# Optimization experiments

Measured on AMD Instinct MI355X. Metric: run time of the kernel, lower is better.

The kernel has to match this reference:

```python
import jax, jax.numpy as jnp
import numpy as np

L, H, D, HD, DFF, V, S, B = 12, 12, 768, 64, 3072, 50257, 512, 4
NEG = -1e10  # mask value used by the torch module (applied incl. diagonal, pre-scale)


def layer_norm(x, g, b, eps=1e-5):
    u = jnp.mean(x, axis=-1, keepdims=True)
    v = jnp.mean((x - u) ** 2, axis=-1, keepdims=True)  # biased variance
    return g * (x - u) / jnp.sqrt(v + eps) + b


def setup_inputs() -> dict:
    key = jax.random.key(0)
    ks = jax.random.split(key, 10)
    f = lambda k, s: 0.02 * jax.random.normal(k, s, dtype=jnp.float32)
    return {
        "tokens": jax.random.randint(ks[0], (B, S), 0, V),
        "E": f(ks[1], (V, D)),
        "P": f(ks[2], (S, D)),
        "Wq": f(ks[3], (L, H, HD, D)),
        "Wk": f(ks[4], (L, H, HD, D)),
        "Wv": f(ks[5], (L, H, HD, D)),
        "Wo": f(ks[6], (L, D, D)),
        "bo": jnp.zeros((L, D), jnp.float32),
        "g1": jnp.ones((L, D), jnp.float32),
        "b1": jnp.zeros((L, D), jnp.float32),
        "g2": jnp.ones((L, D), jnp.float32),
        "b2": jnp.zeros((L, D), jnp.float32),
        "W1": f(ks[7], (L, DFF, D)),
        "bff1": jnp.zeros((L, DFF), jnp.float32),
        "W2": f(ks[8], (L, D, DFF)),
        "bff2": jnp.zeros((L, D), jnp.float32),
        "gf": jnp.ones((D,), jnp.float32),
        "bf": jnp.zeros((D,), jnp.float32),
    }


def reference(tokens, E, P, Wq, Wk, Wv, Wo, bo, g1, b1, g2, b2, W1, bff1, W2, bff2, gf, bf):
    x = E[tokens] + P[None, :, :]  # [B,S,D]; embed_dropout is identity at eval
    # Faithful mask: triu with diagonal=0 (masks the diagonal too), added BEFORE 1/sqrt(dk)
    mask = jnp.triu(jnp.ones((S, S), jnp.float32), k=0) * NEG
    scale = 1.0 / jnp.sqrt(jnp.float32(HD))
    for l in range(L):
        h = layer_norm(x, g1[l], b1[l])
        Q = jnp.einsum('bsd,hkd->bhsk', h, Wq[l])
        K = jnp.einsum('bsd,hkd->bhsk', h, Wk[l])
        Vh = jnp.einsum('bsd,hkd->bhsk', h, Wv[l])
        sc = (jnp.einsum('bhqk,bhmk->bhqm', Q, K) + mask) * scale  # [B,H,S,S]
        A = jax.nn.softmax(sc, axis=-1)
        o = jnp.einsum('bhqm,bhmk->bhqk', A, Vh)  # [B,H,S,HD]
        o = o.transpose(0, 2, 1, 3).reshape(B, S, D)  # concat heads
        x = x + jnp.einsum('bsd,ed->bse', o, Wo[l]) + bo[l]
        h2 = layer_norm(x, g2[l], b2[l])
        ff = jax.nn.gelu(jnp.einsum('bsd,fd->bsf', h2, W1[l]) + bff1[l], approximate=False)
        x = x + jnp.einsum('bsf,df->bsd', ff, W2[l]) + bff2[l]
    x = layer_norm(x, gf, bf)
    return jnp.einsum('bsd,vd->bsv', x, E)  # weight-tied LM head
```

## Files before the change

kernel.cpp:

```cpp
#include <hip/hip_runtime.h>
#include <hip/hip_bf16.h>
#include <math.h>
#include <stdint.h>

#define L      12
#define H      12
#define DMODEL 768
#define HDIM   64
#define DFF    3072
#define VOCAB  50257
#define VPAD2  50432
#define SEQ    512
#define BATCH  4
#define MTOK   2048
#define BKK    64

typedef __hip_bfloat16 bf16;
typedef __bf16 bf16x8 __attribute__((ext_vector_type(8)));
typedef float  f32x4  __attribute__((ext_vector_type(4)));

__device__ inline unsigned int f2bf_bits(float f) {
    __hip_bfloat16 h = __float2bfloat16(f);
    return (unsigned int)__builtin_bit_cast(unsigned short, h);
}

typedef __attribute__((address_space(1))) unsigned int as1_uint;
typedef __attribute__((address_space(3))) unsigned int as3_uint;

__device__ inline void load_lds_16B(const void* g, void* l) {
    __builtin_amdgcn_global_load_lds((as1_uint*)(uintptr_t)g,
                                     (as3_uint*)(uintptr_t)l, 16, 0, 0);
}

__device__ inline int xcd_swz(int raw, int nwg) {
    return (raw & 7) * (nwg >> 3) + (raw >> 3);
}

struct CvtP {
    const float* src[7];
    bf16* dst[7];
    long ns[7];
    long nt[7];
};

__global__ void cvt_all_kernel(CvtP c) {
    long gid0 = ((long)blockIdx.x * blockDim.x + threadIdx.x) * 8;
    long gstr = (long)gridDim.x * blockDim.x * 8;
    for (int s = 0; s < 7; s++) {
        const float* src = c.src[s];
        bf16* dst = c.dst[s];
        long ns = c.ns[s], ntt = c.nt[s];
        for (long i8 = gid0; i8 < ntt; i8 += gstr) {
            uint4 out;
            if (i8 < ns) {
                float4 a = *reinterpret_cast<const float4*>(src + i8);
                float4 b = *reinterpret_cast<const float4*>(src + i8 + 4);
                out.x = f2bf_bits(a.x) | (f2bf_bits(a.y) << 16);
                out.y = f2bf_bits(a.z) | (f2bf_bits(a.w) << 16);
                out.z = f2bf_bits(b.x) | (f2bf_bits(b.y) << 16);
                out.w = f2bf_bits(b.z) | (f2bf_bits(b.w) << 16);
            } else {
                out = (uint4){0u, 0u, 0u, 0u};
            }
            *reinterpret_cast<uint4*>(dst + i8) = out;
        }
    }
}

__global__ __launch_bounds__(256) void embed_ln_kernel(
        float* __restrict__ x, bf16* __restrict__ hout,
        const int* __restrict__ tok, const float* __restrict__ E,
        const float* __restrict__ Pp, const float* __restrict__ g,
        const float* __restrict__ b) {
    int wave = threadIdx.x >> 6, lane = threadIdx.x & 63;
    int row = blockIdx.x * 4 + wave;
    int s = row & (SEQ - 1);
    long ebase = (long)tok[row] * 192;
    const float4* E4 = (const float4*)E;
    const float4* P4 = (const float4*)Pp;
    float4 v[3];
    float s1 = 0.f, s2 = 0.f;
    #pragma unroll
    for (int e = 0; e < 3; e++) {
        int c4 = e * 64 + lane;
        float4 a = E4[ebase + c4];
        float4 p = P4[s * 192 + c4];
        a.x += p.x; a.y += p.y; a.z += p.z; a.w += p.w;
        v[e] = a;
        ((float4*)x)[(size_t)row * 192 + c4] = a;
        s1 += a.x + a.y + a.z + a.w;
        s2 += a.x * a.x + a.y * a.y + a.z * a.z + a.w * a.w;
    }
    #pragma unroll
    for (int o = 32; o > 0; o >>= 1) {
        s1 += __shfl_xor(s1, o);
        s2 += __shfl_xor(s2, o);
    }
    float u    = s1 * (1.f / DMODEL);
    float var  = s2 * (1.f / DMODEL) - u * u;
    float rstd = rsqrtf(var + 1e-5f);
    #pragma unroll
    for (int e = 0; e < 3; e++) {
        int c4 = e * 64 + lane;
        float4 gg = ((const float4*)g)[c4];
        float4 bb = ((const float4*)b)[c4];
        float y0 = gg.x * (v[e].x - u) * rstd + bb.x;
        float y1 = gg.y * (v[e].y - u) * rstd + bb.y;
        float y2 = gg.z * (v[e].z - u) * rstd + bb.z;
        float y3 = gg.w * (v[e].w - u) * rstd + bb.w;
        uint2 o2;
        o2.x = f2bf_bits(y0) | (f2bf_bits(y1) << 16);
        o2.y = f2bf_bits(y2) | (f2bf_bits(y3) << 16);
        ((uint2*)hout)[(size_t)row * 192 + c4] = o2;
    }
}

__global__ __launch_bounds__(256) void reduce_ln_kernel(
        float* __restrict__ x, const float* __restrict__ part, int S,
        const float* __restrict__ bias, const float* __restrict__ g,
        const float* __restrict__ b, bf16* __restrict__ hout) {
    int wave = threadIdx.x >> 6, lane = threadIdx.x & 63;
    int row = blockIdx.x * 4 + wave;
    const float4* part4 = (const float4*)part;
    float4 v[3];
    float s1 = 0.f, s2 = 0.f;
    #pragma unroll
    for (int e = 0; e < 3; e++) {
        int c4 = e * 64 + lane;
        size_t idx = (size_t)row * 192 + c4;
        float4 a = ((const float4*)x)[idx];
        float4 bi = ((const float4*)bias)[c4];
        a.x += bi.x; a.y += bi.y; a.z += bi.z; a.w += bi.w;
        for (int sl = 0; sl < S; sl++) {
            float4 p = part4[((size_t)sl * MTOK + row) * 192 + c4];
            a.x += p.x; a.y += p.y; a.z += p.z; a.w += p.w;
        }
        v[e] = a;
        ((float4*)x)[idx] = a;
        s1 += a.x + a.y + a.z + a.w;
        s2 += a.x * a.x + a.y * a.y + a.z * a.z + a.w * a.w;
    }
    #pragma unroll
    for (int o = 32; o > 0; o >>= 1) {
        s1 += __shfl_xor(s1, o);
        s2 += __shfl_xor(s2, o);
    }
    float u    = s1 * (1.f / DMODEL);
    float var  = s2 * (1.f / DMODEL) - u * u;
    float rstd = rsqrtf(var + 1e-5f);
    #pragma unroll
    for (int e = 0; e < 3; e++) {
        int c4 = e * 64 + lane;
        float4 gg = ((const float4*)g)[c4];
        float4 bb = ((const float4*)b)[c4];
        float y0 = gg.x * (v[e].x - u) * rstd + bb.x;
        float y1 = gg.y * (v[e].y - u) * rstd + bb.y;
        float y2 = gg.z * (v[e].z - u) * rstd + bb.z;
        float y3 = gg.w * (v[e].w - u) * rstd + bb.w;
        uint2 o2;
        o2.x = f2bf_bits(y0) | (f2bf_bits(y1) << 16);
        o2.y = f2bf_bits(y2) | (f2bf_bits(y3) << 16);
        ((uint2*)hout)[(size_t)row * 192 + c4] = o2;
    }
}

#define BM 128

template<int BN_, int EPI>
__global__ __launch_bounds__(256) void gemm_bt(
    const bf16* __restrict__ A, const bf16* __restrict__ Bmat, long strideBz,
    void* __restrict__ Cout, long strideCz,
    const float* __restrict__ bias,
    int Mm, int Nn, int Kk, int Nstore, int kslice)
{
    constexpr int NF = BN_ / 32;
    __shared__ __align__(16) bf16 As[2][BM * BKK];
    __shared__ __align__(16) bf16 Bs[2][BN_ * BKK];
    int tid = threadIdx.x;
    int lane = tid & 63, wave = tid >> 6;

    int Mtiles = Mm / BM;
    int id = xcd_swz(blockIdx.x, gridDim.x);
    int bm = (id % Mtiles) * BM;
    int bn = (id / Mtiles) * BN_;
    int z = blockIdx.z;
    const bf16* Bz = Bmat + (size_t)z * strideBz;
    int wr = (wave >> 1) * 64, wc = (wave & 1) * (BN_ / 2);

    int k0 = (EPI == 4) ? z * kslice : 0;
    int nt = ((EPI == 4) ? kslice : Kk) / BKK;

    f32x4 acc[4][NF];
    #pragma unroll
    for (int i = 0; i < 4; i++)
        #pragma unroll
        for (int j = 0; j < NF; j++) acc[i][j] = (f32x4){0.f, 0.f, 0.f, 0.f};

    auto stage = [&](int slot, int kt) {
        #pragma unroll
        for (int i = 0; i < 4; i++) {
            int byte = i * 4096 + tid * 16;
            int r = byte >> 7;
            int scb = (byte & 127) ^ ((r & 7) << 4);
            load_lds_16B(A + (size_t)(bm + r) * Kk + kt + (scb >> 1),
                         (char*)As[slot] + byte);
        }
        #pragma unroll
        for (int i = 0; i < BN_ / 32; i++) {
            int byte = i * 4096 + tid * 16;
            int r = byte >> 7;
            int scb = (byte & 127) ^ ((r & 7) << 4);
            load_lds_16B(Bz + (size_t)(bn + r) * Kk + kt + (scb >> 1),
                         (char*)Bs[slot] + byte);
        }
    };

    const int swz_rd = (lane & 7) << 4;
    stage(0, k0);
    for (int t = 0; t < nt; ++t) {
        if (t + 1 < nt) {
            stage((t + 1) & 1, k0 + (t + 1) * BKK);
            if constexpr (BN_ == 128) {
                asm volatile("s_waitcnt vmcnt(8)" ::: "memory");
            } else {
                asm volatile("s_waitcnt vmcnt(6)" ::: "memory");
            }
        } else {
            asm volatile("s_waitcnt vmcnt(0)" ::: "memory");
        }
        __builtin_amdgcn_s_barrier();
        __builtin_amdgcn_sched_barrier(0);
        __builtin_amdgcn_s_setprio(1);
        int cur = t & 1;
        #pragma unroll
        for (int kk = 0; kk < 2; ++kk) {
            bf16x8 af[4], bfr[NF];
            int ro = lane & 15;
            int cob = kk * 64 + (lane >> 4) * 16;
            #pragma unroll
            for (int mi = 0; mi < 4; mi++) {
                int row = wr + mi * 16 + ro;
                af[mi] = *reinterpret_cast<const bf16x8*>(
                    (const char*)As[cur] + row * 128 + (cob ^ swz_rd));
            }
            #pragma unroll
            for (int ni = 0; ni < NF; ni++) {
                int row = wc + ni * 16 + ro;
                bfr[ni] = *reinterpret_cast<const bf16x8*>(
                    (const char*)Bs[cur] + row * 128 + (cob ^ swz_rd));
            }
            #pragma unroll
            for (int mi = 0; mi < 4; mi++)
                #pragma unroll
                for (int ni = 0; ni < NF; ni++)
                    acc[mi][ni] = __builtin_amdgcn_mfma_f32_16x16x32_bf16(
                        af[mi], bfr[ni], acc[mi][ni], 0, 0, 0);
        }
        __builtin_amdgcn_s_setprio(0);
        __builtin_amdgcn_s_barrier();
    }

    int rbase = bm + wr + ((lane >> 4) << 2);
    int cbase = bn + wc + (lane & 15);
    #pragma unroll
    for (int mi = 0; mi < 4; mi++) {
        #pragma unroll
        for (int ni = 0; ni < NF; ni++) {
            int col = cbase + ni * 16;
            #pragma unroll
            for (int r = 0; r < 4; r++) {
                int row = rbase + mi * 16 + r;
                float v = acc[mi][ni][r];
                if constexpr (EPI == 0) {
                    ((bf16*)Cout)[(size_t)z * strideCz + (size_t)row * Nn + col] =
                        __float2bfloat16(v);
                } else if constexpr (EPI == 2) {
                    float t2 = v + bias[col];
                    float gel = 0.5f * t2 * (1.f + erff(t2 * 0.70710678118654752f));
                    ((bf16*)Cout)[(size_t)row * Nn + col] = __float2bfloat16(gel);
                } else if constexpr (EPI == 3) {
                    if (col < Nstore)
                        ((float*)Cout)[(size_t)row * Nstore + col] = v;
                } else {
                    ((float*)Cout)[(size_t)z * strideCz + (size_t)row * Nn + col] = v;
                }
            }
        }
    }
}

__global__ void __launch_bounds__(512, 2) gemm_head256(
    const bf16* __restrict__ A, const bf16* __restrict__ Bmat,
    float* __restrict__ Cout, int Nstore)
{
    extern __shared__ char smem[];
    const int Kk = DMODEL;
    const int nt = Kk / BKK;
    int tid = threadIdx.x;
    int lane = tid & 63, wave = tid >> 6;
    int wm = wave >> 1, wn = wave & 1;
    int id = xcd_swz(blockIdx.x, gridDim.x);
    int bm = (id & 7) * 256;
    int bn = (id >> 3) * 128;

    f32x4 acc[4][4];
    #pragma unroll
    for (int i = 0; i < 4; i++)
        #pragma unroll
        for (int j = 0; j < 4; j++) acc[i][j] = (f32x4){0.f, 0.f, 0.f, 0.f};

    auto stage = [&](int slot, int kt) {
        #pragma unroll
        for (int i = 0; i < 4; i++) {
            int byte = i * 8192 + tid * 16;
            int r = byte >> 7;
            int scb = (byte & 127) ^ ((r & 7) << 4);
            load_lds_16B(A + (size_t)(bm + r) * Kk + kt + (scb >> 1),
                         smem + slot * 32768 + byte);
        }
        #pragma unroll
        for (int i = 0; i < 2; i++) {
            int byte = i * 8192 + tid * 16;
            int r = byte >> 7;
            int scb = (byte & 127) ^ ((r & 7) << 4);
            load_lds_16B(Bmat + (size_t)(bn + r) * Kk + kt + (scb >> 1),
                         smem + 98304 + slot * 16384 + byte);
        }
    };

    const int swz_rd = (lane & 7) << 4;
    stage(0, 0);
    stage(1, BKK);
    for (int t = 0; t < nt; ++t) {
        if (t < nt - 1) {
            asm volatile("s_waitcnt vmcnt(6)" ::: "memory");
        } else {
            asm volatile("s_waitcnt vmcnt(0)" ::: "memory");
        }
        __builtin_amdgcn_s_barrier();
        __builtin_amdgcn_sched_barrier(0);
        if (t + 2 < nt) stage((t + 2) % 3, (t + 2) * BKK);
        int cur = t % 3;
        const char* Ab = smem + cur * 32768;
        const char* Bb = smem + 98304 + cur * 16384;
        __builtin_amdgcn_s_setprio(1);
        #pragma unroll
        for (int kk = 0; kk < 2; ++kk) {
            bf16x8 af[4], bfr[4];
            int ro = lane & 15;
            int cob = kk * 64 + (lane >> 4) * 16;
            #pragma unroll
            for (int mi = 0; mi < 4; mi++) {
                int row = wm * 64 + mi * 16 + ro;
                af[mi] = *reinterpret_cast<const bf16x8*>(
                    Ab + row * 128 + (cob ^ swz_rd));
            }
            #pragma unroll
            for (int ni = 0; ni < 4; ni++) {
                int row = wn * 64 + ni * 16 + ro;
                bfr[ni] = *reinterpret_cast<const bf16x8*>(
                    Bb + row * 128 + (cob ^ swz_rd));
            }
            #pragma unroll
            for (int mi = 0; mi < 4; mi++)
                #pragma unroll
                for (int ni = 0; ni < 4; ni++)
                    acc[mi][ni] = __builtin_amdgcn_mfma_f32_16x16x32_bf16(
                        af[mi], bfr[ni], acc[mi][ni], 0, 0, 0);
        }
        __builtin_amdgcn_s_setprio(0);
    }

    int rbase = bm + wm * 64 + ((lane >> 4) << 2);
    int cbase = bn + wn * 64 + (lane & 15);
    #pragma unroll
    for (int mi = 0; mi < 4; mi++) {
        #pragma unroll
        for (int ni = 0; ni < 4; ni++) {
            int col = cbase + ni * 16;
            #pragma unroll
            for (int r = 0; r < 4; r++) {
                int row = rbase + mi * 16 + r;
                if (col < Nstore)
                    Cout[(size_t)row * Nstore + col] = acc[mi][ni][r];
            }
        }
    }
}

#define NEGMASK -1e10f
#define SM_SCALE 0.125f

__global__ __launch_bounds__(256) void attn_kernel(
    bf16* __restrict__ o, const bf16* __restrict__ qb,
    const bf16* __restrict__ kb, const bf16* __restrict__ vb)
{
    __shared__ __align__(16) bf16 K_lds[64 * 64];
    __shared__ __align__(16) bf16 VT_lds[64 * 64];
    __shared__ __align__(16) bf16 P_lds[4][16 * 64];

    int tid = threadIdx.x;
    int wave = tid >> 6, lane = tid & 63;
    int g = lane >> 4;
    int cq = lane & 15;
    int idx = xcd_swz(blockIdx.x, gridDim.x);
    int qt = idx & 7;
    int bh = idx >> 3;
    int h = bh % H, b = bh / H;
    int q0 = qt * 64;
    const size_t base = ((size_t)b * SEQ) * DMODEL + h * HDIM;

    bf16x8 qa[2];
    #pragma unroll
    for (int kk = 0; kk < 2; kk++)
        qa[kk] = *reinterpret_cast<const bf16x8*>(
            qb + base + (size_t)(q0 + wave * 16 + cq) * DMODEL + kk * 32 + g * 8);

    f32x4 acc_o[4];
    #pragma unroll
    for (int df = 0; df < 4; df++) acc_o[df] = (f32x4){0.f, 0.f, 0.f, 0.f};
    float m_run[4] = {-INFINITY, -INFINITY, -INFINITY, -INFINITY};
    float l_run[4] = {0.f, 0.f, 0.f, 0.f};

    int ntiles = (qt == 0) ? (SEQ / 64) : (qt + 1);
    for (int t = 0; t < ntiles; ++t) {
        int mt = t * 64;
        __syncthreads();
        #pragma unroll
        for (int i = 0; i < 2; i++) {
            int byte = i * 4096 + tid * 16;
            int r = byte >> 7;
            int scb = (byte & 127) ^ ((r & 7) << 4);
            load_lds_16B(kb + base + (size_t)(mt + r) * DMODEL + (scb >> 1),
                         (char*)K_lds + byte);
        }
        {
            int rp = tid & 31;
            int c0 = (tid >> 5) * 8;
            const bf16* v0p = vb + base + (size_t)(mt + 2 * rp) * DMODEL + c0;
            uint4 a = *reinterpret_cast<const uint4*>(v0p);
            uint4 bb = *reinterpret_cast<const uint4*>(v0p + DMODEL);
            unsigned int au[4] = {a.x, a.y, a.z, a.w};
            unsigned int bu[4] = {bb.x, bb.y, bb.z, bb.w};
            #pragma unroll
            for (int j = 0; j < 8; j++) {
                unsigned int lo = (j & 1) ? (au[j >> 1] >> 16) : (au[j >> 1] & 0xffffu);
                unsigned int hi = (j & 1) ? (bu[j >> 1] >> 16) : (bu[j >> 1] & 0xffffu);
                int d = c0 + j;
                int byte = d * 128 + ((rp * 4) ^ ((d & 7) << 4));
                *reinterpret_cast<unsigned int*>((char*)VT_lds + byte) = lo | (hi << 16);
            }
        }
        __syncthreads();

        f32x4 s[4];
        #pragma unroll
        for (int nf = 0; nf < 4; nf++) s[nf] = (f32x4){0.f, 0.f, 0.f, 0.f};
        __builtin_amdgcn_s_setprio(1);
        #pragma unroll
        for (int kk = 0; kk < 2; kk++) {
            #pragma unroll
            for (int nf = 0; nf < 4; nf++) {
                int row = nf * 16 + cq;
                bf16x8 kf = *reinterpret_cast<const bf16x8*>(
                    (const char*)K_lds + row * 128 +
                    ((kk * 64 + g * 16) ^ ((row & 7) << 4)));
                s[nf] = __builtin_amdgcn_mfma_f32_16x16x32_bf16(qa[kk], kf, s[nf], 0, 0, 0);
            }
        }
        __builtin_amdgcn_s_setprio(0);

        float p[4][4];
        #pragma unroll
        for (int r = 0; r < 4; r++) {
            int qg = q0 + wave * 16 + (g << 2) + r;
            float sv[4];
            float vmax = -INFINITY;
            #pragma unroll
            for (int nf = 0; nf < 4; nf++) {
                int kv = mt + nf * 16 + cq;
                float d = s[nf][r];
                sv[nf] = (kv >= qg) ? (d + NEGMASK) * SM_SCALE : d * SM_SCALE;
                vmax = fmaxf(vmax, sv[nf]);
            }
            vmax = fmaxf(vmax, __shfl_xor(vmax, 1));
            vmax = fmaxf(vmax, __shfl_xor(vmax, 2));
            vmax = fmaxf(vmax, __shfl_xor(vmax, 4));
            vmax = fmaxf(vmax, __shfl_xor(vmax, 8));
            float nm = fmaxf(m_run[r], vmax);
            float f = __expf(m_run[r] - nm);
            m_run[r] = nm;
            float ps = 0.f;
            #pragma unroll
            for (int nf = 0; nf < 4; nf++) {
                float pv = __expf(sv[nf] - nm);
                p[nf][r] = pv;
                ps += pv;
            }
            ps += __shfl_xor(ps, 1);
            ps += __shfl_xor(ps, 2);
            ps += __shfl_xor(ps, 4);
            ps += __shfl_xor(ps, 8);
            l_run[r] = l_run[r] * f + ps;
            #pragma unroll
            for (int df = 0; df < 4; df++) acc_o[df][r] *= f;
        }

        #pragma unroll
        for (int nf = 0; nf < 4; nf++)
            #pragma unroll
            for (int r = 0; r < 4; r++) {
                int q = (g << 2) + r;
                int blog = nf * 32 + cq * 2;
                int byte = wave * 2048 + q * 128 + (blog ^ ((q & 7) << 4));
                *reinterpret_cast<unsigned short*>((char*)P_lds + byte) =
                    (unsigned short)f2bf_bits(p[nf][r]);
            }
        __syncthreads();

        __builtin_amdgcn_s_setprio(1);
        #pragma unroll
        for (int kk = 0; kk < 2; kk++) {
            bf16x8 pa = *reinterpret_cast<const bf16x8*>(
                (const char*)P_lds + wave * 2048 + cq * 128 +
                ((kk * 64 + g * 16) ^ ((cq & 7) << 4)));
            #pragma unroll
            for (int df = 0; df < 4; df++) {
                int row = df * 16 + cq;
                bf16x8 vf = *reinterpret_cast<const bf16x8*>(
                    (const char*)VT_lds + row * 128 +
                    ((kk * 64 + g * 16) ^ ((row & 7) << 4)));
                acc_o[df] = __builtin_amdgcn_mfma_f32_16x16x32_bf16(pa, vf, acc_o[df], 0, 0, 0);
            }
        }
        __builtin_amdgcn_s_setprio(0);
    }

    #pragma unroll
    for (int r = 0; r < 4; r++) {
        float inv = 1.f / l_run[r];
        int qg = q0 + wave * 16 + (g << 2) + r;
        #pragma unroll
        for (int df = 0; df < 4; df++) {
            o[base + (size_t)qg * DMODEL + df * 16 + cq] =
                __float2bfloat16(acc_o[df][r] * inv);
        }
    }
}

extern "C" void kernel_launch(void* const* d_in, const int* in_sizes, int n_in,
                              void* d_out, int out_size, void* d_ws, size_t ws_size,
                              hipStream_t stream)
{
    (void)in_sizes; (void)n_in; (void)out_size; (void)ws_size;
    const int*   tokens = (const int*)d_in[0];
    const float* E    = (const float*)d_in[1];
    const float* P    = (const float*)d_in[2];
    const float* Wq   = (const float*)d_in[3];
    const float* Wk   = (const float*)d_in[4];
    const float* Wv   = (const float*)d_in[5];
    const float* Wo   = (const float*)d_in[6];
    const float* bo   = (const float*)d_in[7];
    const float* g1   = (const float*)d_in[8];
    const float* b1   = (const float*)d_in[9];
    const float* g2   = (const float*)d_in[10];
    const float* b2   = (const float*)d_in[11];
    const float* W1   = (const float*)d_in[12];
    const float* bff1 = (const float*)d_in[13];
    const float* W2   = (const float*)d_in[14];
    const float* bff2 = (const float*)d_in[15];
    const float* gf   = (const float*)d_in[16];
    const float* bfin = (const float*)d_in[17];

    char* ws = (char*)d_ws;
    size_t off = 0;
    auto alloc = [&](size_t bytes) -> void* {
        void* p = ws + off;
        off += (bytes + 255) & ~(size_t)255;
        return p;
    };
    float* x     = (float*)alloc((size_t)MTOK * DMODEL * 4);
    bf16* hbuf   = (bf16*)alloc((size_t)MTOK * DMODEL * 2);
    bf16* qkv    = (bf16*)alloc((size_t)3 * MTOK * DMODEL * 2);
    bf16* obuf   = (bf16*)alloc((size_t)MTOK * DMODEL * 2);
    bf16* ffb    = (bf16*)alloc((size_t)MTOK * DFF * 2);
    float* part  = (float*)alloc((size_t)3 * MTOK * DMODEL * 4);
    bf16* Eb     = (bf16*)alloc((size_t)VPAD2 * DMODEL * 2);
    bf16* Wqkv_b = (bf16*)alloc((size_t)3 * L * DMODEL * DMODEL * 2);
    bf16* Wo_b   = (bf16*)alloc((size_t)L * DMODEL * DMODEL * 2);
    bf16* W1_b   = (bf16*)alloc((size_t)L * DFF * DMODEL * 2);
    bf16* W2_b   = (bf16*)alloc((size_t)L * DMODEL * DFF * 2);

    long nW = (long)L * DMODEL * DMODEL;
    long nF = (long)L * DFF * DMODEL;
    CvtP cp;
    cp.src[0] = E;  cp.dst[0] = Eb;          cp.ns[0] = (long)VOCAB * DMODEL; cp.nt[0] = (long)VPAD2 * DMODEL;
    cp.src[1] = Wq; cp.dst[1] = Wqkv_b;      cp.ns[1] = nW; cp.nt[1] = nW;
    cp.src[2] = Wk; cp.dst[2] = Wqkv_b + nW; cp.ns[2] = nW; cp.nt[2] = nW;
    cp.src[3] = Wv; cp.dst[3] = Wqkv_b + 2 * nW; cp.ns[3] = nW; cp.nt[3] = nW;
    cp.src[4] = Wo; cp.dst[4] = Wo_b;        cp.ns[4] = nW; cp.nt[4] = nW;
    cp.src[5] = W1; cp.dst[5] = W1_b;        cp.ns[5] = nF; cp.nt[5] = nF;
    cp.src[6] = W2; cp.dst[6] = W2_b;        cp.ns[6] = nF; cp.nt[6] = nF;
    cvt_all_kernel<<<2048, 256, 0, stream>>>(cp);

    embed_ln_kernel<<<MTOK / 4, 256, 0, stream>>>(x, hbuf, tokens, E, P, g1, b1);

    const long pstride = (long)MTOK * DMODEL;
    for (int l = 0; l < L; ++l) {
        gemm_bt<64, 0><<<dim3(192, 1, 3), 256, 0, stream>>>(
            hbuf, Wqkv_b + (size_t)l * DMODEL * DMODEL, nW,
            qkv, pstride, nullptr, MTOK, DMODEL, DMODEL, 0, 0);
        attn_kernel<<<BATCH * H * (SEQ / 64), 256, 0, stream>>>(
            obuf, qkv, qkv + pstride, qkv + 2 * pstride);
        gemm_bt<64, 4><<<dim3(192, 1, 3), 256, 0, stream>>>(
            obuf, Wo_b + (size_t)l * DMODEL * DMODEL, 0,
            part, pstride, nullptr, MTOK, DMODEL, DMODEL, 0, DMODEL / 3);
        reduce_ln_kernel<<<MTOK / 4, 256, 0, stream>>>(
            x, part, 3, bo + l * DMODEL, g2 + l * DMODEL, b2 + l * DMODEL, hbuf);
        gemm_bt<128, 2><<<dim3(16 * 24, 1, 1), 256, 0, stream>>>(
            hbuf, W1_b + (size_t)l * DFF * DMODEL, 0,
            ffb, 0, bff1 + l * DFF, MTOK, DFF, DMODEL, 0, 0);
        gemm_bt<64, 4><<<dim3(192, 1, 3), 256, 0, stream>>>(
            ffb, W2_b + (size_t)l * DMODEL * DFF, 0,
            part, pstride, nullptr, MTOK, DMODEL, DFF, 0, DFF / 3);
        const float* ng = (l < L - 1) ? (g1 + (l + 1) * DMODEL) : gf;
        const float* nb = (l < L - 1) ? (b1 + (l + 1) * DMODEL) : bfin;
        reduce_ln_kernel<<<MTOK / 4, 256, 0, stream>>>(
            x, part, 3, bff2 + l * DMODEL, ng, nb, hbuf);
    }

    (void)hipFuncSetAttribute((const void*)gemm_head256,
        hipFuncAttributeMaxDynamicSharedMemorySize, 147456);
    (void)hipGetLastError();
    gemm_head256<<<dim3(8 * 394), 512, 147456, stream>>>(
        hbuf, Eb, (float*)d_out, VOCAB);
    if (hipGetLastError() != hipSuccess) {
        gemm_bt<128, 3><<<dim3(16 * 394, 1, 1), 256, 0, stream>>>(
            hbuf, Eb, 0, d_out, 0, nullptr, MTOK, VPAD2, DMODEL, VOCAB, 0);
    }
}
```

Baseline: 1.740 ms.

## Interleave LDS reads, global prefetch chunks and MFMA phases in LM-head GEMM

Splits each k-tile of the LM-head GEMM main loop into four phases. Each phase loads a subset of A/B fragments from LDS, issues one chunk of the next stage's global-to-LDS prefetch, then runs half the MFMAs. This spreads memory issue across the compute and lowers fragment register pressure (bfr goes from 4 to 2). In exchange it adds extra workgroup barriers and lgkmcnt waits per tile, which may serialize waves.

```diff
diff --git a/kernel.cpp b/kernel.cpp
--- a/kernel.cpp
+++ b/kernel.cpp
@@ -309,29 +309,46 @@
         #pragma unroll
         for (int j = 0; j < 4; j++) acc[i][j] = (f32x4){0.f, 0.f, 0.f, 0.f};
 
-    auto stage = [&](int slot, int kt) {
-        #pragma unroll
-        for (int i = 0; i < 4; i++) {
-            int byte = i * 8192 + tid * 16;
-            int r = byte >> 7;
-            int scb = (byte & 127) ^ ((r & 7) << 4);
-            load_lds_16B(A + (size_t)(bm + r) * Kk + kt + (scb >> 1),
-                         smem + slot * 32768 + byte);
-        }
-        #pragma unroll
-        for (int i = 0; i < 2; i++) {
-            int byte = i * 8192 + tid * 16;
-            int r = byte >> 7;
-            int scb = (byte & 127) ^ ((r & 7) << 4);
-            load_lds_16B(Bmat + (size_t)(bn + r) * Kk + kt + (scb >> 1),
-                         smem + 98304 + slot * 16384 + byte);
+    auto stage_part = [&](int slot, int kt, int chunk) {
+        if (chunk < 2) {
+            #pragma unroll
+            for (int i = 0; i < 2; i++) {
+                int ii = chunk * 2 + i;
+                int byte = ii * 8192 + tid * 16;
+                int r = byte >> 7;
+                int scb = (byte & 127) ^ ((r & 7) << 4);
+                load_lds_16B(A + (size_t)(bm + r) * Kk + kt + (scb >> 1),
+                             smem + slot * 32768 + byte);
+            }
+        } else {
+            #pragma unroll
+            for (int i = 0; i < 2; i++) {
+                int byte = i * 8192 + tid * 16;
+                int r = byte >> 7;
+                int scb = (byte & 127) ^ ((r & 7) << 4);
+                load_lds_16B(Bmat + (size_t)(bn + r) * Kk + kt + (scb >> 1),
+                             smem + 98304 + slot * 16384 + byte);
+            }
         }
     };
 
     const int swz_rd = (lane & 7) << 4;
-    stage(0, 0);
-    stage(1, BKK);
+    const int ro = lane & 15;
+    stage_part(0, 0, 0); stage_part(0, 0, 1); stage_part(0, 0, 2);
+    stage_part(1, BKK, 0); stage_part(1, BKK, 1); stage_part(1, BKK, 2);
+
     for (int t = 0; t < nt; ++t) {
+        int cur = t % 3;
+        const char* Ab = smem + cur * 32768;
+        const char* Bb = smem + 98304 + cur * 16384;
+        int slot2 = (t + 2) % 3;
+        int kt2 = (t + 2) * BKK;
+        bool pf = (t + 2 < nt);
+
+        bf16x8 af[4], bfr[2];
+        int cob0 = (lane >> 4) * 16;
+        int cob1 = 64 + (lane >> 4) * 16;
+
         if (t < nt - 1) {
             asm volatile("s_waitcnt vmcnt(6)" ::: "memory");
         } else {
@@ -339,35 +356,84 @@
         }
         __builtin_amdgcn_s_barrier();
         __builtin_amdgcn_sched_barrier(0);
-        if (t + 2 < nt) stage((t + 2) % 3, (t + 2) * BKK);
-        int cur = t % 3;
-        const char* Ab = smem + cur * 32768;
-        const char* Bb = smem + 98304 + cur * 16384;
+        #pragma unroll
+        for (int mi = 0; mi < 4; mi++) {
+            int row = wm * 64 + mi * 16 + ro;
+            af[mi] = *reinterpret_cast<const bf16x8*>(Ab + row * 128 + (cob0 ^ swz_rd));
+        }
+        #pragma unroll
+        for (int j = 0; j < 2; j++) {
+            int row = wn * 64 + j * 16 + ro;
+            bfr[j] = *reinterpret_cast<const bf16x8*>(Bb + row * 128 + (cob0 ^ swz_rd));
+        }
+        if (pf) stage_part(slot2, kt2, 0);
+        asm volatile("s_waitcnt lgkmcnt(0)" ::: "memory");
+        __builtin_amdgcn_sched_barrier(0);
         __builtin_amdgcn_s_setprio(1);
         #pragma unroll
-        for (int kk = 0; kk < 2; ++kk) {
-            bf16x8 af[4], bfr[4];
-            int ro = lane & 15;
-            int cob = kk * 64 + (lane >> 4) * 16;
-            #pragma unroll
-            for (int mi = 0; mi < 4; mi++) {
-                int row = wm * 64 + mi * 16 + ro;
-                af[mi] = *reinterpret_cast<const bf16x8*>(
-                    Ab + row * 128 + (cob ^ swz_rd));
-            }
-            #pragma unroll
-            for (int ni = 0; ni < 4; ni++) {
-                int row = wn * 64 + ni * 16 + ro;
-                bfr[ni] = *reinterpret_cast<const bf16x8*>(
-                    Bb + row * 128 + (cob ^ swz_rd));
-            }
-            #pragma unroll
-            for (int mi = 0; mi < 4; mi++)
-                #pragma unroll
-                for (int ni = 0; ni < 4; ni++)
-                    acc[mi][ni] = __builtin_amdgcn_mfma_f32_16x16x32_bf16(
-                        af[mi], bfr[ni], acc[mi][ni], 0, 0, 0);
-        }
+        for (int mi = 0; mi < 4; mi++)
+            #pragma unroll
+            for (int j = 0; j < 2; j++)
+                acc[mi][j] = __builtin_amdgcn_mfma_f32_16x16x32_bf16(
+                    af[mi], bfr[j], acc[mi][j], 0, 0, 0);
+        __builtin_amdgcn_s_setprio(0);
+        __builtin_amdgcn_s_barrier();
+
+        #pragma unroll
+        for (int j = 0; j < 2; j++) {
+            int row = wn * 64 + (2 + j) * 16 + ro;
+            bfr[j] = *reinterpret_cast<const bf16x8*>(Bb + row * 128 + (cob0 ^ swz_rd));
+        }
+        if (pf) stage_part(slot2, kt2, 1);
+        asm volatile("s_waitcnt lgkmcnt(0)" ::: "memory");
+        __builtin_amdgcn_sched_barrier(0);
+        __builtin_amdgcn_s_setprio(1);
+        #pragma unroll
+        for (int mi = 0; mi < 4; mi++)
+            #pragma unroll
+            for (int j = 0; j < 2; j++)
+                acc[mi][2 + j] = __builtin_amdgcn_mfma_f32_16x16x32_bf16(
+                    af[mi], bfr[j], acc[mi][2 + j], 0, 0, 0);
+        __builtin_amdgcn_s_setprio(0);
+        __builtin_amdgcn_s_barrier();
+
+        #pragma unroll
+        for (int mi = 0; mi < 4; mi++) {
+            int row = wm * 64 + mi * 16 + ro;
+            af[mi] = *reinterpret_cast<const bf16x8*>(Ab + row * 128 + (cob1 ^ swz_rd));
+        }
+        #pragma unroll
+        for (int j = 0; j < 2; j++) {
+            int row = wn * 64 + j * 16 + ro;
+            bfr[j] = *reinterpret_cast<const bf16x8*>(Bb + row * 128 + (cob1 ^ swz_rd));
+        }
+        if (pf) stage_part(slot2, kt2, 2);
+        asm volatile("s_waitcnt lgkmcnt(0)" ::: "memory");
+        __builtin_amdgcn_sched_barrier(0);
+        __builtin_amdgcn_s_setprio(1);
+        #pragma unroll
+        for (int mi = 0; mi < 4; mi++)
+            #pragma unroll
+            for (int j = 0; j < 2; j++)
+                acc[mi][j] = __builtin_amdgcn_mfma_f32_16x16x32_bf16(
+                    af[mi], bfr[j], acc[mi][j], 0, 0, 0);
+        __builtin_amdgcn_s_setprio(0);
+        __builtin_amdgcn_s_barrier();
+
+        #pragma unroll
+        for (int j = 0; j < 2; j++) {
+            int row = wn * 64 + (2 + j) * 16 + ro;
+            bfr[j] = *reinterpret_cast<const bf16x8*>(Bb + row * 128 + (cob1 ^ swz_rd));
+        }
+        asm volatile("s_waitcnt lgkmcnt(0)" ::: "memory");
+        __builtin_amdgcn_sched_barrier(0);
+        __builtin_amdgcn_s_setprio(1);
+        #pragma unroll
+        for (int mi = 0; mi < 4; mi++)
+            #pragma unroll
+            for (int j = 0; j < 2; j++)
+                acc[mi][2 + j] = __builtin_amdgcn_mfma_f32_16x16x32_bf16(
+                    af[mi], bfr[j], acc[mi][2 + j], 0, 0, 0);
         __builtin_amdgcn_s_setprio(0);
     }
 
```

Result: no change. 1.736 ms (-0.2%).

## Rework LM head GEMM into 256x256 tiles with quarter-staged ping-pong pipeline

Applied to the files above, without the earlier changes.

Replaces the 256x128-tile LM-head GEMM with a 256x256-tile kernel that splits each K step into four quadrant phases. Each phase issues the next step's A or B half-tile load, syncs with a barrier, then runs MFMAs on the quadrant whose operands are ready. The waves are rearranged 2x4, and the triple-buffered LDS is replaced by double buffering in 128 KB. The aim is to raise arithmetic intensity per tile and interleave global loads with MFMA work, at the cost of more barriers per K step, more accumulator registers, and half as many blocks.

```diff
diff --git a/kernel.cpp b/kernel.cpp
--- a/kernel.cpp
+++ b/kernel.cpp
@@ -289,7 +289,44 @@
     }
 }
 
-__global__ void __launch_bounds__(512, 2) gemm_head256(
+#define H8P_READ_A(mq_)                                                        \
+    _Pragma("unroll")                                                          \
+    for (int mi = 0; mi < 4; mi++) {                                           \
+        int row = wm * 64 + mi * 16 + ro;                                      \
+        _Pragma("unroll")                                                      \
+        for (int kk = 0; kk < 2; kk++) {                                       \
+            af[mq_][mi][kk] = *reinterpret_cast<const bf16x8*>(                \
+                smem + (slot * 2 + mq_) * 16384 + row * 128 +                  \
+                ((kk * 64 + cg16) ^ ((row & 7) << 4)));                        \
+        }                                                                      \
+    }
+
+#define H8P_READ_B(nq_)                                                       \
+    _Pragma("unroll")                                                          \
+    for (int ni = 0; ni < 2; ni++) {                                           \
+        int row = wn * 32 + ni * 16 + ro;                                      \
+        _Pragma("unroll")                                                      \
+        for (int kk = 0; kk < 2; kk++) {                                       \
+            bfr[nq_][ni][kk] = *reinterpret_cast<const bf16x8*>(               \
+                smem + 65536 + (slot * 2 + nq_) * 16384 + row * 128 +          \
+                ((kk * 64 + cg16) ^ ((row & 7) << 4)));                        \
+        }                                                                      \
+    }
+
+#define H8P_MFMA(mq_, nq_)                                                     \
+    __builtin_amdgcn_s_setprio(1);                                             \
+    _Pragma("unroll")                                                          \
+    for (int kk = 0; kk < 2; kk++)                                             \
+        _Pragma("unroll")                                                      \
+        for (int mi = 0; mi < 4; mi++)                                         \
+            _Pragma("unroll")                                                  \
+            for (int ni = 0; ni < 2; ni++)                                     \
+                acc[mq_][nq_][mi][ni] = __builtin_amdgcn_mfma_f32_16x16x32_bf16( \
+                    af[mq_][mi][kk], bfr[nq_][ni][kk], acc[mq_][nq_][mi][ni],  \
+                    0, 0, 0);                                                  \
+    __builtin_amdgcn_s_setprio(0);
+
+__global__ void __launch_bounds__(512, 2) gemm_head8p(
     const bf16* __restrict__ A, const bf16* __restrict__ Bmat,
     float* __restrict__ Cout, int Nstore)
 {
@@ -298,91 +335,109 @@
     const int nt = Kk / BKK;
     int tid = threadIdx.x;
     int lane = tid & 63, wave = tid >> 6;
-    int wm = wave >> 1, wn = wave & 1;
+    int wm = wave >> 2, wn = wave & 3;
     int id = xcd_swz(blockIdx.x, gridDim.x);
     int bm = (id & 7) * 256;
-    int bn = (id >> 3) * 128;
-
-    f32x4 acc[4][4];
-    #pragma unroll
-    for (int i = 0; i < 4; i++)
-        #pragma unroll
-        for (int j = 0; j < 4; j++) acc[i][j] = (f32x4){0.f, 0.f, 0.f, 0.f};
-
-    auto stage = [&](int slot, int kt) {
-        #pragma unroll
-        for (int i = 0; i < 4; i++) {
-            int byte = i * 8192 + tid * 16;
-            int r = byte >> 7;
-            int scb = (byte & 127) ^ ((r & 7) << 4);
-            load_lds_16B(A + (size_t)(bm + r) * Kk + kt + (scb >> 1),
-                         smem + slot * 32768 + byte);
-        }
+    int bn = (id >> 3) * 256;
+    const int ro = lane & 15;
+    const int cg16 = (lane >> 4) * 16;
+
+    f32x4 acc[2][2][4][2];
+    #pragma unroll
+    for (int a0 = 0; a0 < 2; a0++)
+        #pragma unroll
+        for (int a1 = 0; a1 < 2; a1++)
+            #pragma unroll
+            for (int a2 = 0; a2 < 4; a2++)
+                #pragma unroll
+                for (int a3 = 0; a3 < 2; a3++)
+                    acc[a0][a1][a2][a3] = (f32x4){0.f, 0.f, 0.f, 0.f};
+
+    bf16x8 af[2][4][2];
+    bf16x8 bfr[2][2][2];
+
+    auto stage_half = [&](int slot_, int kt, int which) {
+        int h = which >> 1;
         #pragma unroll
         for (int i = 0; i < 2; i++) {
             int byte = i * 8192 + tid * 16;
             int r = byte >> 7;
             int scb = (byte & 127) ^ ((r & 7) << 4);
-            load_lds_16B(Bmat + (size_t)(bn + r) * Kk + kt + (scb >> 1),
-                         smem + 98304 + slot * 16384 + byte);
+            if ((which & 1) == 0)
+                load_lds_16B(A + (size_t)(bm + h * 128 + r) * Kk + kt + (scb >> 1),
+                             smem + (slot_ * 2 + h) * 16384 + byte);
+            else
+                load_lds_16B(Bmat + (size_t)(bn + h * 128 + r) * Kk + kt + (scb >> 1),
+                             smem + 65536 + (slot_ * 2 + h) * 16384 + byte);
         }
     };
 
-    const int swz_rd = (lane & 7) << 4;
-    stage(0, 0);
-    stage(1, BKK);
-    for (int t = 0; t < nt; ++t) {
-        if (t < nt - 1) {
-            asm volatile("s_waitcnt vmcnt(6)" ::: "memory");
+    stage_half(0, 0, 0); stage_half(0, 0, 1); stage_half(0, 0, 2); stage_half(0, 0, 3);
+
+    for (int k = 0; k < nt; ++k) {
+        int slot = k & 1, nslot = slot ^ 1;
+        int kt2 = (k + 1) * BKK;
+        bool pf = (k + 1 < nt);
+
+        asm volatile("s_waitcnt vmcnt(4)" ::: "memory");
+        if (pf) stage_half(nslot, kt2, 0);
+        __builtin_amdgcn_s_barrier();
+        __builtin_amdgcn_sched_barrier(0);
+        H8P_READ_A(0)
+        H8P_READ_B(0)
+        asm volatile("s_waitcnt lgkmcnt(0)" ::: "memory");
+        __builtin_amdgcn_sched_barrier(0);
+        H8P_MFMA(0, 0)
+
+        if (pf) {
+            asm volatile("s_waitcnt vmcnt(4)" ::: "memory");
+        } else {
+            asm volatile("s_waitcnt vmcnt(2)" ::: "memory");
+        }
+        if (pf) stage_half(nslot, kt2, 1);
+        __builtin_amdgcn_s_barrier();
+        __builtin_amdgcn_sched_barrier(0);
+        H8P_READ_A(1)
+        asm volatile("s_waitcnt lgkmcnt(0)" ::: "memory");
+        __builtin_amdgcn_sched_barrier(0);
+        H8P_MFMA(1, 0)
+
+        if (pf) {
+            asm volatile("s_waitcnt vmcnt(4)" ::: "memory");
         } else {
             asm volatile("s_waitcnt vmcnt(0)" ::: "memory");
         }
+        if (pf) stage_half(nslot, kt2, 2);
         __builtin_amdgcn_s_barrier();
         __builtin_amdgcn_sched_barrier(0);
-        if (t + 2 < nt) stage((t + 2) % 3, (t + 2) * BKK);
-        int cur = t % 3;
-        const char* Ab = smem + cur * 32768;
-        const char* Bb = smem + 98304 + cur * 16384;
-        __builtin_amdgcn_s_setprio(1);
-        #pragma unroll
-        for (int kk = 0; kk < 2; ++kk) {
-            bf16x8 af[4], bfr[4];
-            int ro = lane & 15;
-            int cob = kk * 64 + (lane >> 4) * 16;
+        H8P_READ_B(1)
+        asm volatile("s_waitcnt lgkmcnt(0)" ::: "memory");
+        __builtin_amdgcn_sched_barrier(0);
+        H8P_MFMA(0, 1)
+
+        if (pf) stage_half(nslot, kt2, 3);
+        __builtin_amdgcn_s_barrier();
+        __builtin_amdgcn_sched_barrier(0);
+        H8P_MFMA(1, 1)
+    }
+
+    #pragma unroll
+    for (int mq = 0; mq < 2; mq++) {
+        #pragma unroll
+        for (int nq = 0; nq < 2; nq++) {
             #pragma unroll
             for (int mi = 0; mi < 4; mi++) {
-                int row = wm * 64 + mi * 16 + ro;
-                af[mi] = *reinterpret_cast<const bf16x8*>(
-                    Ab + row * 128 + (cob ^ swz_rd));
-            }
-            #pragma unroll
-            for (int ni = 0; ni < 4; ni++) {
-                int row = wn * 64 + ni * 16 + ro;
-                bfr[ni] = *reinterpret_cast<const bf16x8*>(
-                    Bb + row * 128 + (cob ^ swz_rd));
-            }
-            #pragma unroll
-            for (int mi = 0; mi < 4; mi++)
                 #pragma unroll
-                for (int ni = 0; ni < 4; ni++)
-                    acc[mi][ni] = __builtin_amdgcn_mfma_f32_16x16x32_bf16(
-                        af[mi], bfr[ni], acc[mi][ni], 0, 0, 0);
-        }
-        __builtin_amdgcn_s_setprio(0);
-    }
-
-    int rbase = bm + wm * 64 + ((lane >> 4) << 2);
-    int cbase = bn + wn * 64 + (lane & 15);
-    #pragma unroll
-    for (int mi = 0; mi < 4; mi++) {
-        #pragma unroll
-        for (int ni = 0; ni < 4; ni++) {
-            int col = cbase + ni * 16;
-            #pragma unroll
-            for (int r = 0; r < 4; r++) {
-                int row = rbase + mi * 16 + r;
-                if (col < Nstore)
-                    Cout[(size_t)row * Nstore + col] = acc[mi][ni][r];
+                for (int ni = 0; ni < 2; ni++) {
+                    int col = bn + nq * 128 + wn * 32 + ni * 16 + (lane & 15);
+                    #pragma unroll
+                    for (int r = 0; r < 4; r++) {
+                        int row = bm + mq * 128 + wm * 64 + mi * 16 +
+                                  ((lane >> 4) << 2) + r;
+                        if (col < Nstore)
+                            Cout[(size_t)row * Nstore + col] = acc[mq][nq][mi][ni][r];
+                    }
+                }
             }
         }
     }
@@ -629,10 +684,10 @@
             x, part, 3, bff2 + l * DMODEL, ng, nb, hbuf);
     }
 
-    (void)hipFuncSetAttribute((const void*)gemm_head256,
-        hipFuncAttributeMaxDynamicSharedMemorySize, 147456);
+    (void)hipFuncSetAttribute((const void*)gemm_head8p,
+        hipFuncAttributeMaxDynamicSharedMemorySize, 131072);
     (void)hipGetLastError();
-    gemm_head256<<<dim3(8 * 394), 512, 147456, stream>>>(
+    gemm_head8p<<<dim3(8 * 197), 512, 131072, stream>>>(
         hbuf, Eb, (float*)d_out, VOCAB);
     if (hipGetLastError() != hipSuccess) {
         gemm_bt<128, 3><<<dim3(16 * 394, 1, 1), 256, 0, stream>>>(
```

After: 1.703 ms. 1.02x faster.
